# Kernel optimization log

Measured on AMD Instinct MI355X. Metric: run time of the kernel, lower is better.

Reference implementation:

```python
import jax, jax.numpy as jnp
import numpy as np

N_NODES = 100000

def gcn_conv(x, edge_index, W, b):
    # normalize=False GCNConv: out[i] = sum_{(j->i) in E} (x W)[j] + b
    h = x @ W                                   # [N, out_dim]
    src, dst = edge_index[0], edge_index[1]
    msgs = h[src]                               # [E, out_dim]
    agg = jax.ops.segment_sum(msgs, dst, num_segments=N_NODES)
    return agg + b

def setup_inputs() -> dict:
    key = jax.random.key(0)
    k1, k2, k3, k4 = jax.random.split(key, 4)
    x = jax.random.normal(k1, (N_NODES, 512), dtype=jnp.float32)
    edge_index = jax.random.randint(k2, (2, 3200000), 0, N_NODES, dtype=jnp.int64)
    W1 = jax.random.normal(k3, (512, 16), dtype=jnp.float32) * (1.0 / np.sqrt(512))
    b1 = jnp.zeros((16,), dtype=jnp.float32)
    W2 = jax.random.normal(k4, (16, 40), dtype=jnp.float32) * (1.0 / np.sqrt(16))
    b2 = jnp.zeros((40,), dtype=jnp.float32)
    return {"x": x, "edge_index": edge_index, "W1": W1, "b1": b1, "W2": W2, "b2": b2}

def reference(x, edge_index, W1, b1, W2, b2):
    h = jax.nn.relu(gcn_conv(x, edge_index, W1, b1))
    # dropout is identity at inference (training=False)
    out = gcn_conv(h, edge_index, W2, b2)
    return jax.nn.log_softmax(out, axis=1)
```

## Files before the change

kernel.cpp:

```cpp
#include <hip/hip_runtime.h>
#include <math.h>

#define N_NODES 100000
#define N_EDGES 3200000
#define BSHIFT 7
#define BNODES 128
#define NB 782
#define PLACE_BLOCKS 400

__global__ __launch_bounds__(256) void gemm1_kernel(
    const float* __restrict__ x, const float* __restrict__ W1,
    float* __restrict__ h, int nrows)
{
    __shared__ float xs[32 * 260];
    const int t = threadIdx.x;
    const int rbase = blockIdx.x * 256;
    const int rq = t >> 2;
    const int cg = t & 3;

    float4 acc0 = make_float4(0.f, 0.f, 0.f, 0.f);
    float4 acc1 = acc0, acc2 = acc0, acc3 = acc0;

    const int kl4  = (t & 7) * 4;
    const int rstg = t >> 3;
    const float4* w4 = (const float4*)W1;

    for (int kc = 0; kc < 512; kc += 32) {
        #pragma unroll
        for (int i = 0; i < 8; ++i) {
            int row = rstg + i * 32;
            int rg  = rbase + row;
            float4 v = make_float4(0.f, 0.f, 0.f, 0.f);
            if (rg < nrows)
                v = *(const float4*)(x + (size_t)rg * 512 + kc + kl4);
            xs[(kl4 + 0) * 260 + row] = v.x;
            xs[(kl4 + 1) * 260 + row] = v.y;
            xs[(kl4 + 2) * 260 + row] = v.z;
            xs[(kl4 + 3) * 260 + row] = v.w;
        }
        __syncthreads();

        #pragma unroll
        for (int k4 = 0; k4 < 8; ++k4) {
            const int k0 = k4 * 4;
            float4 xv0 = *(const float4*)(xs + (k0 + 0) * 260 + rq * 4);
            float4 xv1 = *(const float4*)(xs + (k0 + 1) * 260 + rq * 4);
            float4 xv2 = *(const float4*)(xs + (k0 + 2) * 260 + rq * 4);
            float4 xv3 = *(const float4*)(xs + (k0 + 3) * 260 + rq * 4);
            float4 wv0 = w4[(kc + k0 + 0) * 4 + cg];
            float4 wv1 = w4[(kc + k0 + 1) * 4 + cg];
            float4 wv2 = w4[(kc + k0 + 2) * 4 + cg];
            float4 wv3 = w4[(kc + k0 + 3) * 4 + cg];

            #define GCN_UPD(xv, wv)                                           \
                acc0.x += (xv).x * (wv).x; acc0.y += (xv).x * (wv).y;         \
                acc0.z += (xv).x * (wv).z; acc0.w += (xv).x * (wv).w;         \
                acc1.x += (xv).y * (wv).x; acc1.y += (xv).y * (wv).y;         \
                acc1.z += (xv).y * (wv).z; acc1.w += (xv).y * (wv).w;         \
                acc2.x += (xv).z * (wv).x; acc2.y += (xv).z * (wv).y;         \
                acc2.z += (xv).z * (wv).z; acc2.w += (xv).z * (wv).w;         \
                acc3.x += (xv).w * (wv).x; acc3.y += (xv).w * (wv).y;         \
                acc3.z += (xv).w * (wv).z; acc3.w += (xv).w * (wv).w;
            GCN_UPD(xv0, wv0)
            GCN_UPD(xv1, wv1)
            GCN_UPD(xv2, wv2)
            GCN_UPD(xv3, wv3)
            #undef GCN_UPD
        }
        __syncthreads();
    }
    {
        int rg = rbase + rq * 4;
        if (rg + 0 < nrows) *(float4*)(h + (size_t)(rg + 0) * 16 + cg * 4) = acc0;
        if (rg + 1 < nrows) *(float4*)(h + (size_t)(rg + 1) * 16 + cg * 4) = acc1;
        if (rg + 2 < nrows) *(float4*)(h + (size_t)(rg + 2) * 16 + cg * 4) = acc2;
        if (rg + 3 < nrows) *(float4*)(h + (size_t)(rg + 3) * 16 + cg * 4) = acc3;
    }
}

__global__ __launch_bounds__(256) void bin_count_kernel(
    const int* __restrict__ ei, int* __restrict__ bucket_cnt)
{
    __shared__ int hist[NB];
    const int t = threadIdx.x;
    for (int i = t; i < NB; i += 256) hist[i] = 0;
    __syncthreads();
    const int stride = gridDim.x * 256;
    for (int e = blockIdx.x * 256 + t; e < N_EDGES; e += stride)
        atomicAdd(&hist[ei[N_EDGES + e] >> BSHIFT], 1);
    __syncthreads();
    for (int i = t; i < NB; i += 256)
        if (hist[i]) atomicAdd(&bucket_cnt[i], hist[i]);
}

__global__ __launch_bounds__(1024) void bucket_scan_kernel(
    const int* __restrict__ bucket_cnt, int* __restrict__ bucket_base,
    int* __restrict__ bucket_cursor)
{
    __shared__ int s[1024];
    const int t = threadIdx.x;
    s[t] = (t < NB) ? bucket_cnt[t] : 0;
    __syncthreads();
    for (int off = 1; off < 1024; off <<= 1) {
        int v = (t >= off) ? s[t - off] : 0;
        __syncthreads();
        s[t] += v;
        __syncthreads();
    }
    if (t < NB) {
        int excl = (t == 0) ? 0 : s[t - 1];
        bucket_base[t]   = excl;
        bucket_cursor[t] = excl;
        if (t == NB - 1) bucket_base[NB] = s[t];
    }
}

__global__ __launch_bounds__(256) void bin_place_kernel(
    const int* __restrict__ ei, int* __restrict__ bucket_cursor,
    int* __restrict__ packed)
{
    __shared__ int cnt[NB];
    __shared__ int base_off[NB];
    __shared__ int cur[NB];
    const int t = threadIdx.x;
    const int chunk = (N_EDGES + PLACE_BLOCKS - 1) / PLACE_BLOCKS;
    const int cs = blockIdx.x * chunk;
    const int ce = min(cs + chunk, N_EDGES);

    for (int i = t; i < NB; i += 256) { cnt[i] = 0; cur[i] = 0; }
    __syncthreads();
    for (int e = cs + t; e < ce; e += 256)
        atomicAdd(&cnt[ei[N_EDGES + e] >> BSHIFT], 1);
    __syncthreads();
    for (int i = t; i < NB; i += 256)
        base_off[i] = cnt[i] ? atomicAdd(&bucket_cursor[i], cnt[i]) : 0;
    __syncthreads();
    for (int e = cs + t; e < ce; e += 256) {
        int s = ei[e];
        int d = ei[N_EDGES + e];
        int b = d >> BSHIFT;
        int pos = base_off[b] + atomicAdd(&cur[b], 1);
        packed[pos] = s | ((d & (BNODES - 1)) << 17);
    }
}

__global__ __launch_bounds__(256) void csr_sort_kernel(
    const int* __restrict__ bucket_base, const int* __restrict__ packed,
    int* __restrict__ csr_src, int* __restrict__ row_ptr)
{
    __shared__ int hist[BNODES];
    __shared__ int excl[BNODES];
    __shared__ int cur[BNODES];
    __shared__ int scan[BNODES];
    const int t = threadIdx.x;
    const int b = blockIdx.x;
    if (t < BNODES) { hist[t] = 0; cur[t] = 0; }
    __syncthreads();

    const int bs = bucket_base[b];
    const int be = bucket_base[b + 1];
    for (int e = bs + t; e < be; e += 256)
        atomicAdd(&hist[packed[e] >> 17], 1);
    __syncthreads();

    if (t < BNODES) scan[t] = hist[t];
    __syncthreads();
    for (int off = 1; off < BNODES; off <<= 1) {
        int v = (t < BNODES && t >= off) ? scan[t - off] : 0;
        __syncthreads();
        if (t < BNODES) scan[t] += v;
        __syncthreads();
    }
    if (t < BNODES) {
        int ex = (t == 0) ? 0 : scan[t - 1];
        excl[t] = ex;
        int g = b * BNODES + t;
        if (g < N_NODES) row_ptr[g] = bs + ex;
    }
    if (b == NB - 1 && t == 0) row_ptr[N_NODES] = N_EDGES;
    __syncthreads();

    for (int e = bs + t; e < be; e += 256) {
        int p  = packed[e];
        int dl = p >> 17;
        int pos = bs + excl[dl] + atomicAdd(&cur[dl], 1);
        csr_src[pos] = p & 0x1FFFF;
    }
}

__global__ __launch_bounds__(256) void gather1_kernel(
    const int* __restrict__ row_ptr, const int* __restrict__ csr_src,
    const float* __restrict__ h, const float* __restrict__ b1,
    float* __restrict__ h1)
{
    const int node = (blockIdx.x * 256 + threadIdx.x) >> 6;
    if (node >= N_NODES) return;
    const int lane = threadIdx.x & 63;
    const int c = lane & 15, slot = lane >> 4;
    const int start = row_ptr[node], end = row_ptr[node + 1];

    float acc = 0.f;
    int e = start;
    for (; e + 16 <= end; e += 16) {
        int s0 = csr_src[e + slot * 4 + 0];
        int s1 = csr_src[e + slot * 4 + 1];
        int s2 = csr_src[e + slot * 4 + 2];
        int s3 = csr_src[e + slot * 4 + 3];
        float v0 = h[s0 * 16 + c];
        float v1 = h[s1 * 16 + c];
        float v2 = h[s2 * 16 + c];
        float v3 = h[s3 * 16 + c];
        acc += (v0 + v1) + (v2 + v3);
    }
    for (; e + 4 <= end; e += 4)
        acc += h[csr_src[e + slot] * 16 + c];
    if (e + slot < end)
        acc += h[csr_src[e + slot] * 16 + c];

    acc += __shfl_xor(acc, 16);
    acc += __shfl_xor(acc, 32);
    if (lane < 16)
        h1[(size_t)node * 16 + c] = fmaxf(acc + b1[c], 0.f);
}

__global__ __launch_bounds__(256) void gather2_kernel(
    const int* __restrict__ row_ptr, const int* __restrict__ csr_src,
    const float* __restrict__ h1, const float* __restrict__ W2,
    const float* __restrict__ b2, float* __restrict__ out)
{
    const int node = (blockIdx.x * 256 + threadIdx.x) >> 6;
    if (node >= N_NODES) return;
    const int lane = threadIdx.x & 63;
    const int c = lane & 15, slot = lane >> 4;

    float w2c[16];
    float b2v = 0.f;
    if (lane < 40) {
        b2v = b2[lane];
        #pragma unroll
        for (int k = 0; k < 16; ++k) w2c[k] = W2[k * 40 + lane];
    } else {
        #pragma unroll
        for (int k = 0; k < 16; ++k) w2c[k] = 0.f;
    }

    const int start = row_ptr[node], end = row_ptr[node + 1];
    float acc = 0.f;
    int e = start;
    for (; e + 16 <= end; e += 16) {
        int s0 = csr_src[e + slot * 4 + 0];
        int s1 = csr_src[e + slot * 4 + 1];
        int s2 = csr_src[e + slot * 4 + 2];
        int s3 = csr_src[e + slot * 4 + 3];
        float v0 = h1[s0 * 16 + c];
        float v1 = h1[s1 * 16 + c];
        float v2 = h1[s2 * 16 + c];
        float v3 = h1[s3 * 16 + c];
        acc += (v0 + v1) + (v2 + v3);
    }
    for (; e + 4 <= end; e += 4)
        acc += h1[csr_src[e + slot] * 16 + c];
    if (e + slot < end)
        acc += h1[csr_src[e + slot] * 16 + c];

    acc += __shfl_xor(acc, 16);
    acc += __shfl_xor(acc, 32);

    float z = b2v;
    #pragma unroll
    for (int k = 0; k < 16; ++k)
        z += __shfl(acc, k) * w2c[k];

    float zm = (lane < 40) ? z : -1e30f;
    #pragma unroll
    for (int off = 1; off < 64; off <<= 1)
        zm = fmaxf(zm, __shfl_xor(zm, off));
    float ex = (lane < 40) ? __expf(z - zm) : 0.f;
    float sum = ex;
    #pragma unroll
    for (int off = 1; off < 64; off <<= 1)
        sum += __shfl_xor(sum, off);
    const float lse = zm + __logf(sum);

    if (lane < 40)
        out[(size_t)node * 40 + lane] = z - lse;
}

extern "C" void kernel_launch(void* const* d_in, const int* in_sizes, int n_in,
                              void* d_out, int out_size, void* d_ws, size_t ws_size,
                              hipStream_t stream)
{
    const float* x  = (const float*)d_in[0];
    const int*   ei = (const int*)d_in[1];
    const float* W1 = (const float*)d_in[2];
    const float* b1 = (const float*)d_in[3];
    const float* W2 = (const float*)d_in[4];
    const float* b2 = (const float*)d_in[5];
    float* out = (float*)d_out;

    float* h      = (float*)d_ws;
    int*   csr    = (int*)(h + (size_t)N_NODES * 16);
    int*   packed = csr + N_EDGES;
    float* h1     = (float*)packed;
    int*   rowp   = packed + N_EDGES;
    int*   bcnt   = rowp + (N_NODES + 1);
    int*   bbase  = bcnt + NB;
    int*   bcur   = bbase + (NB + 1);

    const int node_blocks   = (N_NODES + 255) / 256;
    const int gather_blocks = (N_NODES + 3) / 4;

    hipMemsetAsync(bcnt, 0, NB * sizeof(int), stream);
    bin_count_kernel  <<<256, 256, 0, stream>>>(ei, bcnt);
    bucket_scan_kernel<<<1, 1024, 0, stream>>>(bcnt, bbase, bcur);
    bin_place_kernel  <<<PLACE_BLOCKS, 256, 0, stream>>>(ei, bcur, packed);
    csr_sort_kernel   <<<NB, 256, 0, stream>>>(bbase, packed, csr, rowp);

    gemm1_kernel<<<node_blocks, 256, 0, stream>>>(x, W1, h, N_NODES);

    gather1_kernel<<<gather_blocks, 256, 0, stream>>>(rowp, csr, h, b1, h1);
    gather2_kernel<<<gather_blocks, 256, 0, stream>>>(rowp, csr, h1, W2, b2, out);
}
```

Before: 605.0 us.

## Replace shared-memory tiled GEMM1 with direct per-row register dot products

```diff
diff --git a/kernel.cpp b/kernel.cpp
--- a/kernel.cpp
+++ b/kernel.cpp
@@ -12,70 +12,31 @@
     const float* __restrict__ x, const float* __restrict__ W1,
     float* __restrict__ h, int nrows)
 {
-    __shared__ float xs[32 * 260];
-    const int t = threadIdx.x;
-    const int rbase = blockIdx.x * 256;
+    const int t = threadIdx.x;
     const int rq = t >> 2;
     const int cg = t & 3;
-
-    float4 acc0 = make_float4(0.f, 0.f, 0.f, 0.f);
-    float4 acc1 = acc0, acc2 = acc0, acc3 = acc0;
-
-    const int kl4  = (t & 7) * 4;
-    const int rstg = t >> 3;
-    const float4* w4 = (const float4*)W1;
-
-    for (int kc = 0; kc < 512; kc += 32) {
-        #pragma unroll
-        for (int i = 0; i < 8; ++i) {
-            int row = rstg + i * 32;
-            int rg  = rbase + row;
-            float4 v = make_float4(0.f, 0.f, 0.f, 0.f);
-            if (rg < nrows)
-                v = *(const float4*)(x + (size_t)rg * 512 + kc + kl4);
-            xs[(kl4 + 0) * 260 + row] = v.x;
-            xs[(kl4 + 1) * 260 + row] = v.y;
-            xs[(kl4 + 2) * 260 + row] = v.z;
-            xs[(kl4 + 3) * 260 + row] = v.w;
-        }
-        __syncthreads();
-
-        #pragma unroll
-        for (int k4 = 0; k4 < 8; ++k4) {
-            const int k0 = k4 * 4;
-            float4 xv0 = *(const float4*)(xs + (k0 + 0) * 260 + rq * 4);
-            float4 xv1 = *(const float4*)(xs + (k0 + 1) * 260 + rq * 4);
-            float4 xv2 = *(const float4*)(xs + (k0 + 2) * 260 + rq * 4);
-            float4 xv3 = *(const float4*)(xs + (k0 + 3) * 260 + rq * 4);
-            float4 wv0 = w4[(kc + k0 + 0) * 4 + cg];
-            float4 wv1 = w4[(kc + k0 + 1) * 4 + cg];
-            float4 wv2 = w4[(kc + k0 + 2) * 4 + cg];
-            float4 wv3 = w4[(kc + k0 + 3) * 4 + cg];
-
-            #define GCN_UPD(xv, wv)                                           \
-                acc0.x += (xv).x * (wv).x; acc0.y += (xv).x * (wv).y;         \
-                acc0.z += (xv).x * (wv).z; acc0.w += (xv).x * (wv).w;         \
-                acc1.x += (xv).y * (wv).x; acc1.y += (xv).y * (wv).y;         \
-                acc1.z += (xv).y * (wv).z; acc1.w += (xv).y * (wv).w;         \
-                acc2.x += (xv).z * (wv).x; acc2.y += (xv).z * (wv).y;         \
-                acc2.z += (xv).z * (wv).z; acc2.w += (xv).z * (wv).w;         \
-                acc3.x += (xv).w * (wv).x; acc3.y += (xv).w * (wv).y;         \
-                acc3.z += (xv).w * (wv).z; acc3.w += (xv).w * (wv).w;
-            GCN_UPD(xv0, wv0)
-            GCN_UPD(xv1, wv1)
-            GCN_UPD(xv2, wv2)
-            GCN_UPD(xv3, wv3)
-            #undef GCN_UPD
-        }
-        __syncthreads();
-    }
-    {
-        int rg = rbase + rq * 4;
-        if (rg + 0 < nrows) *(float4*)(h + (size_t)(rg + 0) * 16 + cg * 4) = acc0;
-        if (rg + 1 < nrows) *(float4*)(h + (size_t)(rg + 1) * 16 + cg * 4) = acc1;
-        if (rg + 2 < nrows) *(float4*)(h + (size_t)(rg + 2) * 16 + cg * 4) = acc2;
-        if (rg + 3 < nrows) *(float4*)(h + (size_t)(rg + 3) * 16 + cg * 4) = acc3;
-    }
+    const int row = blockIdx.x * 64 + rq;
+    if (row >= nrows) return;
+
+    const float4* __restrict__ w4 = (const float4*)W1;
+    const float4* __restrict__ xr = (const float4*)(x + (size_t)row * 512);
+
+    float4 acc = make_float4(0.f, 0.f, 0.f, 0.f);
+
+    #pragma unroll 4
+    for (int k4 = 0; k4 < 128; ++k4) {
+        float4 xv = xr[k4];
+        float4 w0 = w4[(k4 * 4 + 0) * 4 + cg];
+        float4 w1 = w4[(k4 * 4 + 1) * 4 + cg];
+        float4 w2 = w4[(k4 * 4 + 2) * 4 + cg];
+        float4 w3 = w4[(k4 * 4 + 3) * 4 + cg];
+        acc.x += xv.x * w0.x + xv.y * w1.x + xv.z * w2.x + xv.w * w3.x;
+        acc.y += xv.x * w0.y + xv.y * w1.y + xv.z * w2.y + xv.w * w3.y;
+        acc.z += xv.x * w0.z + xv.y * w1.z + xv.z * w2.z + xv.w * w3.z;
+        acc.w += xv.x * w0.w + xv.y * w1.w + xv.z * w2.w + xv.w * w3.w;
+    }
+
+    *(float4*)(h + (size_t)row * 16 + cg * 4) = acc;
 }
 
 __global__ __launch_bounds__(256) void bin_count_kernel(
@@ -307,7 +268,7 @@
     int*   bbase  = bcnt + NB;
     int*   bcur   = bbase + (NB + 1);
 
-    const int node_blocks   = (N_NODES + 255) / 256;
+    const int gemm1_blocks  = (N_NODES + 63) / 64;
     const int gather_blocks = (N_NODES + 3) / 4;
 
     hipMemsetAsync(bcnt, 0, NB * sizeof(int), stream);
@@ -316,7 +277,7 @@
     bin_place_kernel  <<<PLACE_BLOCKS, 256, 0, stream>>>(ei, bcur, packed);
     csr_sort_kernel   <<<NB, 256, 0, stream>>>(bbase, packed, csr, rowp);
 
-    gemm1_kernel<<<node_blocks, 256, 0, stream>>>(x, W1, h, N_NODES);
+    gemm1_kernel<<<gemm1_blocks, 256, 0, stream>>>(x, W1, h, N_NODES);
 
     gather1_kernel<<<gather_blocks, 256, 0, stream>>>(rowp, csr, h, b1, h1);
     gather2_kernel<<<gather_blocks, 256, 0, stream>>>(rowp, csr, h1, W2, b2, out);
```

After: 662.2 us. +9.5%, slower.

## Restructure gemm1 as single-wave blocks with register prefetch and swizzled LDS

Applied to the files above, without the earlier changes.

```diff
diff --git a/kernel.cpp b/kernel.cpp
--- a/kernel.cpp
+++ b/kernel.cpp
@@ -7,46 +7,68 @@
 #define BNODES 128
 #define NB 782
 #define PLACE_BLOCKS 400
-
-__global__ __launch_bounds__(256) void gemm1_kernel(
+#define G1_S 68
+
+typedef float vfloat4 __attribute__((ext_vector_type(4)));
+
+__global__ __launch_bounds__(64) void gemm1_kernel(
     const float* __restrict__ x, const float* __restrict__ W1,
     float* __restrict__ h, int nrows)
 {
-    __shared__ float xs[32 * 260];
-    const int t = threadIdx.x;
-    const int rbase = blockIdx.x * 256;
+    __shared__ __align__(16) float xs[32 * G1_S];
+    const int t = threadIdx.x;
+    const int rbase = blockIdx.x * 64;
+
+    const int kl4  = (t & 7) * 4;
+    const int rstg = t >> 3;
+    const int swz  = (t & 7) << 3;
+
     const int rq = t >> 2;
     const int cg = t & 3;
+    const float4* __restrict__ w4 = (const float4*)W1;
 
     float4 acc0 = make_float4(0.f, 0.f, 0.f, 0.f);
     float4 acc1 = acc0, acc2 = acc0, acc3 = acc0;
 
-    const int kl4  = (t & 7) * 4;
-    const int rstg = t >> 3;
-    const float4* w4 = (const float4*)W1;
+    vfloat4 pre[8];
+    #pragma unroll
+    for (int i = 0; i < 8; ++i) {
+        int rg = rbase + rstg + i * 8;
+        pre[i] = (rg < nrows)
+            ? __builtin_nontemporal_load(
+                  (const vfloat4*)(x + (size_t)rg * 512 + kl4))
+            : (vfloat4){0.f, 0.f, 0.f, 0.f};
+    }
 
     for (int kc = 0; kc < 512; kc += 32) {
         #pragma unroll
         for (int i = 0; i < 8; ++i) {
-            int row = rstg + i * 32;
-            int rg  = rbase + row;
-            float4 v = make_float4(0.f, 0.f, 0.f, 0.f);
-            if (rg < nrows)
-                v = *(const float4*)(x + (size_t)rg * 512 + kc + kl4);
-            xs[(kl4 + 0) * 260 + row] = v.x;
-            xs[(kl4 + 1) * 260 + row] = v.y;
-            xs[(kl4 + 2) * 260 + row] = v.z;
-            xs[(kl4 + 3) * 260 + row] = v.w;
+            int row = (rstg + i * 8) ^ swz;
+            float* p = xs + kl4 * G1_S + row;
+            p[0 * G1_S] = pre[i].x;
+            p[1 * G1_S] = pre[i].y;
+            p[2 * G1_S] = pre[i].z;
+            p[3 * G1_S] = pre[i].w;
         }
-        __syncthreads();
+        if (kc + 32 < 512) {
+            #pragma unroll
+            for (int i = 0; i < 8; ++i) {
+                int rg = rbase + rstg + i * 8;
+                pre[i] = (rg < nrows)
+                    ? __builtin_nontemporal_load(
+                          (const vfloat4*)(x + (size_t)rg * 512 + kc + 32 + kl4))
+                    : (vfloat4){0.f, 0.f, 0.f, 0.f};
+            }
+        }
 
         #pragma unroll
         for (int k4 = 0; k4 < 8; ++k4) {
             const int k0 = k4 * 4;
-            float4 xv0 = *(const float4*)(xs + (k0 + 0) * 260 + rq * 4);
-            float4 xv1 = *(const float4*)(xs + (k0 + 1) * 260 + rq * 4);
-            float4 xv2 = *(const float4*)(xs + (k0 + 2) * 260 + rq * 4);
-            float4 xv3 = *(const float4*)(xs + (k0 + 3) * 260 + rq * 4);
+            const int rr = (rq * 4) ^ (k4 << 3);
+            float4 xv0 = *(const float4*)(xs + (k0 + 0) * G1_S + rr);
+            float4 xv1 = *(const float4*)(xs + (k0 + 1) * G1_S + rr);
+            float4 xv2 = *(const float4*)(xs + (k0 + 2) * G1_S + rr);
+            float4 xv3 = *(const float4*)(xs + (k0 + 3) * G1_S + rr);
             float4 wv0 = w4[(kc + k0 + 0) * 4 + cg];
             float4 wv1 = w4[(kc + k0 + 1) * 4 + cg];
             float4 wv2 = w4[(kc + k0 + 2) * 4 + cg];
@@ -67,8 +89,8 @@
             GCN_UPD(xv3, wv3)
             #undef GCN_UPD
         }
-        __syncthreads();
-    }
+    }
+
     {
         int rg = rbase + rq * 4;
         if (rg + 0 < nrows) *(float4*)(h + (size_t)(rg + 0) * 16 + cg * 4) = acc0;
@@ -307,7 +329,7 @@
     int*   bbase  = bcnt + NB;
     int*   bcur   = bbase + (NB + 1);
 
-    const int node_blocks   = (N_NODES + 255) / 256;
+    const int gemm1_blocks  = (N_NODES + 63) / 64;
     const int gather_blocks = (N_NODES + 3) / 4;
 
     hipMemsetAsync(bcnt, 0, NB * sizeof(int), stream);
@@ -316,7 +338,7 @@
     bin_place_kernel  <<<PLACE_BLOCKS, 256, 0, stream>>>(ei, bcur, packed);
     csr_sort_kernel   <<<NB, 256, 0, stream>>>(bbase, packed, csr, rowp);
 
-    gemm1_kernel<<<node_blocks, 256, 0, stream>>>(x, W1, h, N_NODES);
+    gemm1_kernel<<<gemm1_blocks, 64, 0, stream>>>(x, W1, h, N_NODES);
 
     gather1_kernel<<<gather_blocks, 256, 0, stream>>>(rowp, csr, h, b1, h1);
     gather2_kernel<<<gather_blocks, 256, 0, stream>>>(rowp, csr, h1, W2, b2, out);
```

After: 545.3 us. -9.9%, faster.
